# Kernel tuning notes

Measured on AMD Instinct MI355X. Metric: run time of the kernel, lower is better.

Reference implementation:

```python
import jax, jax.numpy as jnp
import numpy as np

B, F, H, LAT = 4, 64, 128, 512
N_CALLS = 16          # n_calls=2, module multiplies by 8
NEG = 0.2             # leaky-relu slope
EPS = 1e-5            # InstanceNorm2d eps

# hypernetwork output layout: w_in[F,3F], b_in[F], w_mid[F,F], b_mid[F], w_out[F,F], b_out[F], w_short[F,3F], b_short[F]
_sizes = [3*F*F, F, F*F, F, F*F, F, 3*F*F, F]
_off = np.cumsum([0] + _sizes)
HYP_OUT = int(_off[-1])


def _sobel_kernel():
    # SinSobel: smoothing (cos) x derivative (sin) separable 5x5 gradient filters
    lin = np.linspace(-1.0, 1.0, 5)
    d = np.sin(lin * np.pi / 2.0)
    s = np.cos(lin * np.pi / 2.0)
    gx = np.outer(s, d)                      # d/dx
    gy = np.outer(d, s)                      # d/dy
    k = np.stack([gx, gy])[:, None]          # [2,1,5,5]
    return jnp.asarray(np.tile(k, (F, 1, 1, 1)), jnp.float32)  # [2F,1,5,5] depthwise


def _conv(x, w, pad, groups=1):
    return jax.lax.conv_general_dilated(
        x, w, (1, 1), [(pad, pad), (pad, pad)],
        dimension_numbers=('NCHW', 'OIHW', 'NCHW'),
        feature_group_count=groups)


def _lrelu(x):
    return jnp.where(x >= 0, x, NEG * x)


def setup_inputs() -> dict:
    key = jax.random.key(0)
    ks = jax.random.split(key, 8)
    f32 = jnp.float32
    return {
        "lat": jax.random.normal(ks[0], (B, LAT), f32),
        "ca_init": jax.random.normal(ks[1], (B, F, H, H), f32),
        "leak_factor": jnp.asarray(0.1, f32),
        "hyper_w": jax.random.normal(ks[2], (HYP_OUT, LAT), f32) * 0.02,
        "hyper_b": jnp.zeros((HYP_OUT,), f32),
        "res_w1": jax.random.normal(ks[3], (F, F, 3, 3), f32) * 0.05,
        "res_b1": jnp.zeros((F,), f32),
        "res_w2": jax.random.normal(ks[4], (F, F, 3, 3), f32) * 0.05,
        "res_b2": jnp.zeros((F,), f32),
        "img_w": jax.random.normal(ks[5], (3, F, 3, 3), f32) * 0.05,
        "img_b": jnp.zeros((3,), f32),
    }


def reference(lat, ca_init, leak_factor, hyper_w, hyper_b,
              res_w1, res_b1, res_w2, res_b2, img_w, img_b):
    sob = _sobel_kernel()
    lf = jnp.clip(leak_factor, 0.001, 1000.0)

    # per-sample dynamic 1x1-conv weights from hypernetwork (lat is loop-invariant)
    ws = lat @ hyper_w.T + hyper_b           # [B, HYP_OUT]

    def seg(i, shape):
        return ws[:, _off[i]:_off[i + 1]].reshape((B,) + shape)
    w_in,  b_in  = seg(0, (F, 3 * F)), seg(1, (F,))
    w_mid, b_mid = seg(2, (F, F)),     seg(3, (F,))
    w_out, b_out = seg(4, (F, F)),     seg(5, (F,))
    w_sh,  b_sh  = seg(6, (F, 3 * F)), seg(7, (F,))

    def step(out, _):
        # SinSobel: identity channels + depthwise 5x5 gradients -> [B,3F,H,H]
        y = jnp.concatenate([out, _conv(out, sob, 2, groups=F)], axis=1)
        # InstanceNorm2d (affine=False)
        mu = y.mean((2, 3), keepdims=True)
        var = y.var((2, 3), keepdims=True)
        y = (y - mu) * jax.lax.rsqrt(var + EPS)
        # DynaResidualBlock: per-sample 1x1 convs (batched GEMMs) + shortcut
        h = _lrelu(jnp.einsum('bchw,boc->bohw', y, w_in) + b_in[:, :, None, None])
        h = _lrelu(jnp.einsum('bchw,boc->bohw', h, w_mid) + b_mid[:, :, None, None])
        h = jnp.einsum('bchw,boc->bohw', h, w_out) + b_out[:, :, None, None]
        sc = jnp.einsum('bchw,boc->bohw', y, w_sh) + b_sh[:, :, None, None]
        return out + lf * (h + sc), None

    out, _ = jax.lax.scan(step, ca_init, None, length=N_CALLS)

    # conv_img: ResidualBlock(3x3) then final 3x3 conv to image channels, clamp
    h = _lrelu(_conv(out, res_w1, 1) + res_b1[None, :, None, None])
    h = _conv(h, res_w2, 1) + res_b2[None, :, None, None]
    out = out + h
    img = _conv(out, img_w, 1) + img_b[None, :, None, None]
    return jnp.clip(img, -1.0, 1.0)
```

## Files before the change

kernel.cpp:

```cpp
#include <hip/hip_runtime.h>
#include <cstddef>

#define R_ 0.70710678118654752f
#define NEG_ 0.2f
#define EPS_ 1e-5f

constexpr int F_ = 64, C3_ = 192, HH_ = 128, NPIX_ = 16384, B_ = 4, LAT_ = 512, HYP_ = 33024;
constexpr int OFFI_WIN = 0, OFFI_BIN = 12288, OFFI_WMID = 12352, OFFI_BMID = 16448,
              OFFI_WOUT = 16512, OFFI_BOUT = 20608, OFFI_WSH = 20672, OFFI_BSH = 32960;
constexpr size_t OFF_HYP = 0;
constexpr size_t OFF_SRAW = 134144;
constexpr size_t OFF_WFIN = 140288;
constexpr size_t OFF_WFSH = 189440;
constexpr size_t OFF_WFMID = 238592;
constexpr size_t OFF_WFOUT = 254976;
constexpr size_t OFF_CW1 = 271360;
constexpr size_t OFF_CW2 = 308224;
constexpr size_t OFF_CWIMG = 345088;
constexpr size_t OFF_OUT = 346816;
constexpr size_t OFF_SOB = 4541120;
constexpr size_t OFF_TMP = OFF_SOB;

typedef short bf16x8 __attribute__((ext_vector_type(8)));
typedef float f32x4 __attribute__((ext_vector_type(4)));

static __device__ __forceinline__ unsigned short f2b(float v) {
  unsigned u = __builtin_bit_cast(unsigned, v);
  u += 0x7fffu + ((u >> 16) & 1u);
  return (unsigned short)(u >> 16);
}
static __device__ __forceinline__ float b2f(unsigned short h) {
  return __builtin_bit_cast(float, ((unsigned)h) << 16);
}
static __device__ __forceinline__ void split2(float v, unsigned short& hi, unsigned short& lo) {
  hi = f2b(v);
  lo = f2b(v - b2f(hi));
}

#define MM3(acc, ahi, alo, whi, wlo)                                        \
  acc = __builtin_amdgcn_mfma_f32_16x16x32_bf16(ahi, whi, acc, 0, 0, 0);    \
  acc = __builtin_amdgcn_mfma_f32_16x16x32_bf16(ahi, wlo, acc, 0, 0, 0);    \
  acc = __builtin_amdgcn_mfma_f32_16x16x32_bf16(alo, whi, acc, 0, 0, 0);

__global__ __launch_bounds__(256) void hyper_gemm_kernel(
    const float* __restrict__ lat, const float* __restrict__ hw,
    const float* __restrict__ hb, float* __restrict__ hyp) {
  __shared__ float slat[B_ * LAT_];
  const int tid = threadIdx.x;
  for (int i = tid; i < B_ * LAT_; i += 256) slat[i] = lat[i];
  __syncthreads();
  const int wave = tid >> 6, lane = tid & 63;
  const int j = blockIdx.x * 4 + wave;
  if (j >= HYP_) return;
  const float* wr = hw + (size_t)j * LAT_;
  float a0 = 0.f, a1 = 0.f, a2 = 0.f, a3 = 0.f;
  for (int i = 0; i < LAT_; i += 64) {
    float w = wr[i + lane];
    a0 = __builtin_fmaf(w, slat[0 * LAT_ + i + lane], a0);
    a1 = __builtin_fmaf(w, slat[1 * LAT_ + i + lane], a1);
    a2 = __builtin_fmaf(w, slat[2 * LAT_ + i + lane], a2);
    a3 = __builtin_fmaf(w, slat[3 * LAT_ + i + lane], a3);
  }
  #pragma unroll
  for (int off = 32; off; off >>= 1) {
    a0 += __shfl_down(a0, off, 64);
    a1 += __shfl_down(a1, off, 64);
    a2 += __shfl_down(a2, off, 64);
    a3 += __shfl_down(a3, off, 64);
  }
  if (lane == 0) {
    float b = hb[j];
    hyp[0 * HYP_ + j] = a0 + b;
    hyp[1 * HYP_ + j] = a1 + b;
    hyp[2 * HYP_ + j] = a2 + b;
    hyp[3 * HYP_ + j] = a3 + b;
  }
}

__global__ __launch_bounds__(256) void prep_dynw_kernel(float* wsm) {
  const int b = blockIdx.x >> 3, sl = blockIdx.x & 7;
  const int tid = threadIdx.x;
  const float* hyp = wsm + OFF_HYP + (size_t)b * HYP_;
  unsigned short* wfin = (unsigned short*)(wsm + OFF_WFIN) + (size_t)b * 24576;
  unsigned short* wfsh = (unsigned short*)(wsm + OFF_WFSH) + (size_t)b * 24576;
  unsigned short* wfmid = (unsigned short*)(wsm + OFF_WFMID) + (size_t)b * 8192;
  unsigned short* wfout = (unsigned short*)(wsm + OFF_WFOUT) + (size_t)b * 8192;

  if (sl < 6) {
    const int base = sl * 2048;
    for (int i = tid; i < 2048; i += 256) {
      int idx = base + i;
      int j = idx & 7, ch = (idx >> 3) & 63, g2 = (idx >> 9) & 3, ks = idx >> 11;
      int k = ks * 32 + g2 * 8 + j;
      int fbx = ((ks * 4 + g2) * 64 + ch) * 16;
      unsigned short h, l;
      split2(hyp[OFFI_WIN + ch * C3_ + k], h, l);
      wfin[fbx + j] = h; wfin[fbx + 8 + j] = l;
      split2(hyp[OFFI_WSH + ch * C3_ + k], h, l);
      wfsh[fbx + j] = h; wfsh[fbx + 8 + j] = l;
    }
  } else if (sl == 6) {
    for (int idx = tid; idx < 4096; idx += 256) {
      int j = idx & 7, ch = (idx >> 3) & 63, g2 = (idx >> 9) & 3, ks = idx >> 11;
      int k = ks * 32 + g2 * 8 + j;
      int fbx = ((ks * 4 + g2) * 64 + ch) * 16;
      unsigned short h, l;
      split2(hyp[OFFI_WMID + ch * 64 + k], h, l);
      wfmid[fbx + j] = h; wfmid[fbx + 8 + j] = l;
      split2(hyp[OFFI_WOUT + ch * 64 + k], h, l);
      wfout[fbx + j] = h; wfout[fbx + 8 + j] = l;
    }
  }
}

__global__ __launch_bounds__(256) void prep_convw_kernel(
    const float* __restrict__ w1, const float* __restrict__ w2,
    const float* __restrict__ wi, unsigned short* __restrict__ wf1,
    unsigned short* __restrict__ wf2, float* __restrict__ wit) {
  const int idx = blockIdx.x * 256 + threadIdx.x;
  if (idx < 36864) {
    int j = idx & 7, ch = (idx >> 3) & 63, fg = idx >> 9;
    int k = (fg >> 2) * 32 + (fg & 3) * 8 + j;
    int c = k & 63, t = k >> 6;
    int fb = (fg * 64 + ch) * 16;
    unsigned short h, l;
    split2(w1[(ch * 64 + c) * 9 + t], h, l);
    wf1[fb + j] = h; wf1[fb + 8 + j] = l;
    split2(w2[(ch * 64 + c) * 9 + t], h, l);
    wf2[fb + j] = h; wf2[fb + 8 + j] = l;
  }
  if (idx < 64 * 9 * 3) {
    int k = idx % 3, rest = idx / 3;
    int t = rest % 9, c = rest / 9;
    wit[idx] = wi[(k * 64 + c) * 9 + t];
  }
}

__device__ __forceinline__ float blockReduceSum(float v, float* scratch) {
  const int tid = threadIdx.x;
  #pragma unroll
  for (int off = 32; off; off >>= 1) v += __shfl_down(v, off, 64);
  if ((tid & 63) == 0) scratch[tid >> 6] = v;
  __syncthreads();
  float r = scratch[0] + scratch[1] + scratch[2] + scratch[3];
  __syncthreads();
  return r;
}

__device__ __forceinline__ void hline_z(const float* __restrict__ P, int rr, int col,
                                        float& hdv, float& hsv, float& cv) {
  if (rr < 0 || rr > 127) { hdv = 0.f; hsv = 0.f; cv = 0.f; return; }
  const float* rp = P + rr * HH_;
  float vm2 = (col >= 2) ? rp[col - 2] : 0.f;
  float vm1 = (col >= 1) ? rp[col - 1] : 0.f;
  float v0 = rp[col];
  float vp1 = (col <= 126) ? rp[col + 1] : 0.f;
  float vp2 = (col <= 125) ? rp[col + 2] : 0.f;
  hdv = -vm2 - R_ * vm1 + R_ * vp1 + vp2;
  hsv = R_ * vm1 + v0 + R_ * vp1;
  cv = v0;
}

__global__ __launch_bounds__(256) void sobel_stats_kernel(
    const float* __restrict__ outb, unsigned int* __restrict__ sob,
    float* __restrict__ sraw) {
  __shared__ float scr[4];
  const int bi = blockIdx.x;
  const int q = bi & 3, c = (bi >> 2) & 63, b = bi >> 8;
  const int tid = threadIdx.x;
  const int col = tid & 127;
  const int r0 = q * 32 + (tid >> 7) * 16;
  const float* P = outb + ((size_t)(b * F_ + c)) * NPIX_;
  unsigned int* ygx = sob + ((size_t)(b * 128 + 2 * c)) * NPIX_;
  unsigned int* ygy = ygx + NPIX_;

  float sI = 0.f, qI = 0.f, sX = 0.f, qX = 0.f, sY = 0.f, qY = 0.f;
  float hd_m1, hd_0, hd_p1, hs_m2, hs_m1, hs_0, hs_p1;
  float td, tc;
  hline_z(P, r0 - 2, col, td, hs_m2, tc);
  hline_z(P, r0 - 1, col, hd_m1, hs_m1, tc);
  hline_z(P, r0, col, hd_0, hs_0, tc);
  sI += tc; qI += tc * tc;
  hline_z(P, r0 + 1, col, hd_p1, hs_p1, tc);
  sI += tc; qI += tc * tc;

  for (int i = 0; i < 16; ++i) {
    const int r = r0 + i;
    const int nr = r + 2;
    float hd_new, hs_new, cnew;
    hline_z(P, nr, col, hd_new, hs_new, cnew);
    if (nr <= r0 + 15) { sI += cnew; qI += cnew * cnew; }
    float gxv = R_ * (hd_m1 + hd_p1) + hd_0;
    float gyv = -hs_m2 - R_ * hs_m1 + R_ * hs_p1 + hs_new;
    const int o = r * HH_ + col;
    unsigned short h, l;
    split2(gxv, h, l);
    ygx[o] = ((unsigned)h << 16) | l;
    split2(gyv, h, l);
    ygy[o] = ((unsigned)h << 16) | l;
    sX += gxv; qX += gxv * gxv;
    sY += gyv; qY += gyv * gyv;
    hd_m1 = hd_0; hd_0 = hd_p1; hd_p1 = hd_new;
    hs_m2 = hs_m1; hs_m1 = hs_0; hs_0 = hs_p1; hs_p1 = hs_new;
  }
  __syncthreads();
  float tI = blockReduceSum(sI, scr);
  float tQI = blockReduceSum(qI, scr);
  float tX = blockReduceSum(sX, scr);
  float tQX = blockReduceSum(qX, scr);
  float tY = blockReduceSum(sY, scr);
  float tQY = blockReduceSum(qY, scr);
  if (tid == 0) {
    float* r = sraw + (size_t)bi * 6;
    r[0] = tI; r[1] = tQI; r[2] = tX; r[3] = tQX; r[4] = tY; r[5] = tQY;
  }
}

__global__ __launch_bounds__(256, 2) void mlp_mfma_kernel(
    float* __restrict__ outb, const unsigned int* __restrict__ sobu,
    const float* __restrict__ wsf, const float* __restrict__ leak) {
  __shared__ unsigned short yhi[64 * 200];
  __shared__ unsigned short ylo[64 * 200];
  __shared__ unsigned short hhi[64 * 72];
  __shared__ unsigned short hlo[64 * 72];
  __shared__ unsigned short resb[64 * 66];
  __shared__ float stl[C3_ * 2];
  __shared__ float ssig[64];
  const int bi = blockIdx.x;
  const int b = bi >> 8, t = bi & 255;
  const int px0 = t * 64;
  const int tid = threadIdx.x;

  const float* ob = outb + (size_t)b * F_ * NPIX_;
  const unsigned int* sbp = sobu + (size_t)b * 128 * NPIX_;
  uint4 vbuf[12];
  #pragma unroll
  for (int it = 0; it < 12; ++it) {
    const int ci = it * 256 + tid;
    const int k = ci >> 4, pq = ci & 15;
    const unsigned int* src =
        (k < 64) ? (const unsigned int*)(ob + (size_t)k * NPIX_ + px0 + pq * 4)
                 : (sbp + (size_t)(k - 64) * NPIX_ + px0 + pq * 4);
    vbuf[it] = *(const uint4*)src;
  }

  if (tid < 64) {
    const int c = tid;
    const float* r = wsf + OFF_SRAW + ((size_t)(b * 64 + c) * 4) * 6;
    float sI = 0.f, qI = 0.f, sX = 0.f, qX = 0.f, sY = 0.f, qY = 0.f;
    #pragma unroll
    for (int q = 0; q < 4; ++q) {
      sI += r[q * 6 + 0]; qI += r[q * 6 + 1];
      sX += r[q * 6 + 2]; qX += r[q * 6 + 3];
      sY += r[q * 6 + 4]; qY += r[q * 6 + 5];
    }
    const float n = 1.f / 16384.f;
    float m, rs;
    m = sI * n; rs = rsqrtf(qI * n - m * m + EPS_);
    stl[c * 2] = m; stl[c * 2 + 1] = rs; ssig[c] = 1.f / rs;
    const int cx = 64 + 2 * c, cy = cx + 1;
    m = sX * n; stl[cx * 2] = m;          stl[cx * 2 + 1] = rsqrtf(qX * n - m * m + EPS_);
    m = sY * n; stl[cy * 2] = m;          stl[cy * 2 + 1] = rsqrtf(qY * n - m * m + EPS_);
  }
  __syncthreads();

  #pragma unroll
  for (int it = 0; it < 12; ++it) {
    const int ci = it * 256 + tid;
    const int k = ci >> 4, pq = ci & 15;
    const int kk = k ^ ((pq >> 1) << 3);
    unsigned short* ph = &yhi[(pq * 4) * 200 + kk];
    unsigned short* pl = &ylo[(pq * 4) * 200 + kk];
    const float mu = stl[k * 2], inv = stl[k * 2 + 1];
    const uint4 v = vbuf[it];
    if (k < 64) {
      const float sg = ssig[k];
      const float vv[4] = {__builtin_bit_cast(float, v.x), __builtin_bit_cast(float, v.y),
                           __builtin_bit_cast(float, v.z), __builtin_bit_cast(float, v.w)};
      #pragma unroll
      for (int e = 0; e < 4; ++e) {
        unsigned short h, l;
        split2((vv[e] - mu) * inv, h, l);
        ph[e * 200] = h; pl[e * 200] = l;
        float rec = __builtin_fmaf(b2f(h) + b2f(l), sg, mu);
        resb[k * 66 + pq * 4 + e] = f2b(vv[e] - rec);
      }
    } else {
      const unsigned uu[4] = {v.x, v.y, v.z, v.w};
      #pragma unroll
      for (int e = 0; e < 4; ++e) {
        float val = b2f((unsigned short)(uu[e] >> 16)) + b2f((unsigned short)(uu[e] & 0xffff));
        unsigned short h, l;
        split2((val - mu) * inv, h, l);
        ph[e * 200] = h; pl[e * 200] = l;
      }
    }
  }
  __syncthreads();

  const int wave = tid >> 6, lane = tid & 63;
  const int lrow = lane & 15, g = lane >> 4;
  const int chm = wave * 16 + lrow;
  const float lf = fminf(fmaxf(leak[0], 0.001f), 1000.f);
  const float* hyp = wsf + OFF_HYP + (size_t)b * HYP_;
  const unsigned short* wfin = (const unsigned short*)(wsf + OFF_WFIN) + (size_t)b * 24576;
  const unsigned short* wfsh = (const unsigned short*)(wsf + OFF_WFSH) + (size_t)b * 24576;
  const unsigned short* wfmid = (const unsigned short*)(wsf + OFF_WFMID) + (size_t)b * 8192;
  const unsigned short* wfout = (const unsigned short*)(wsf + OFF_WFOUT) + (size_t)b * 8192;

  f32x4 aH[4], aS[4];
  {
    float b1 = hyp[OFFI_BIN + chm], b2 = hyp[OFFI_BSH + chm];
    #pragma unroll
    for (int pf = 0; pf < 4; ++pf) {
      aH[pf] = (f32x4){b1, b1, b1, b1};
      aS[pf] = (f32x4){b2, b2, b2, b2};
    }
  }
  #pragma unroll
  for (int ks = 0; ks < 6; ++ks) {
    const size_t wo = (size_t)((ks * 4 + g) * 64 + chm) * 16;
    bf16x8 whiI = *(const bf16x8*)(wfin + wo);
    bf16x8 wloI = *(const bf16x8*)(wfin + wo + 8);
    bf16x8 whiS = *(const bf16x8*)(wfsh + wo);
    bf16x8 wloS = *(const bf16x8*)(wfsh + wo + 8);
    #pragma unroll
    for (int pf = 0; pf < 4; ++pf) {
      const int pxl = pf * 16 + lrow;
      const int kb = pxl * 200 + ((ks * 32 + g * 8) ^ ((pxl >> 3) << 3));
      bf16x8 ahi = *(const bf16x8*)&yhi[kb];
      bf16x8 alo = *(const bf16x8*)&ylo[kb];
      MM3(aH[pf], ahi, alo, whiI, wloI);
      MM3(aS[pf], ahi, alo, whiS, wloS);
    }
  }
  #pragma unroll
  for (int pf = 0; pf < 4; ++pf) {
    #pragma unroll
    for (int j = 0; j < 4; ++j) {
      float v = aH[pf][j];
      v = (v >= 0.f) ? v : NEG_ * v;
      unsigned short h, l;
      split2(v, h, l);
      const int o = (pf * 16 + g * 4 + j) * 72 + chm;
      hhi[o] = h; hlo[o] = l;
    }
  }
  __syncthreads();
  f32x4 aM[4];
  {
    float bm = hyp[OFFI_BMID + chm];
    #pragma unroll
    for (int pf = 0; pf < 4; ++pf) aM[pf] = (f32x4){bm, bm, bm, bm};
  }
  #pragma unroll
  for (int ks = 0; ks < 2; ++ks) {
    const size_t wo = (size_t)((ks * 4 + g) * 64 + chm) * 16;
    bf16x8 whi = *(const bf16x8*)(wfmid + wo);
    bf16x8 wlo = *(const bf16x8*)(wfmid + wo + 8);
    #pragma unroll
    for (int pf = 0; pf < 4; ++pf) {
      const int kb = (pf * 16 + lrow) * 72 + ks * 32 + g * 8;
      bf16x8 ahi = *(const bf16x8*)&hhi[kb];
      bf16x8 alo = *(const bf16x8*)&hlo[kb];
      MM3(aM[pf], ahi, alo, whi, wlo);
    }
  }
  __syncthreads();
  #pragma unroll
  for (int pf = 0; pf < 4; ++pf) {
    #pragma unroll
    for (int j = 0; j < 4; ++j) {
      float v = aM[pf][j];
      v = (v >= 0.f) ? v : NEG_ * v;
      unsigned short h, l;
      split2(v, h, l);
      const int o = (pf * 16 + g * 4 + j) * 72 + chm;
      hhi[o] = h; hlo[o] = l;
    }
  }
  __syncthreads();
  f32x4 aO[4];
  {
    float bo = hyp[OFFI_BOUT + chm];
    #pragma unroll
    for (int pf = 0; pf < 4; ++pf) aO[pf] = (f32x4){bo, bo, bo, bo};
  }
  #pragma unroll
  for (int ks = 0; ks < 2; ++ks) {
    const size_t wo = (size_t)((ks * 4 + g) * 64 + chm) * 16;
    bf16x8 whi = *(const bf16x8*)(wfout + wo);
    bf16x8 wlo = *(const bf16x8*)(wfout + wo + 8);
    #pragma unroll
    for (int pf = 0; pf < 4; ++pf) {
      const int kb = (pf * 16 + lrow) * 72 + ks * 32 + g * 8;
      bf16x8 ahi = *(const bf16x8*)&hhi[kb];
      bf16x8 alo = *(const bf16x8*)&hlo[kb];
      MM3(aO[pf], ahi, alo, whi, wlo);
    }
  }
  const float mu_c = stl[chm * 2];
  const float sg_c = ssig[chm];
  #pragma unroll
  for (int pf = 0; pf < 4; ++pf) {
    float* op = outb + ((size_t)(b * F_ + chm)) * NPIX_ + px0 + pf * 16 + g * 4;
    f32x4 nv;
    #pragma unroll
    for (int j = 0; j < 4; ++j) {
      const int pxl = pf * 16 + g * 4 + j;
      const int kk2 = chm ^ ((pxl >> 3) << 3);
      float yv = b2f(yhi[pxl * 200 + kk2]) + b2f(ylo[pxl * 200 + kk2]);
      float vorig = __builtin_fmaf(yv, sg_c, mu_c) + b2f(resb[chm * 66 + pxl]);
      nv[j] = vorig + lf * (aO[pf][j] + aS[pf][j]);
    }
    *(f32x4*)op = nv;
  }
}

__global__ __launch_bounds__(256, 2) void conv_mfma_kernel(
    const float* __restrict__ in, const unsigned short* __restrict__ wf,
    const float* __restrict__ bias, float* __restrict__ dst, int mode) {
  __shared__ unsigned short ahi[4 * 72 * 64];
  __shared__ unsigned short alo[4 * 72 * 64];
  const int bi = blockIdx.x;
  const int b = bi >> 7, rest = bi & 127;
  const int row0 = (rest >> 1) * 2, colbase = (rest & 1) << 6;
  const int tid = threadIdx.x;
  const float* ip = in + (size_t)b * F_ * NPIX_;

  for (int idx = tid; idx < 4608; idx += 256) {
    const int chunk = idx % 18;
    const int rowp = (idx / 18) % 4;
    const int ch = idx / 72;
    const int r2 = row0 - 1 + rowp;
    const int gcol0 = colbase - 4 + chunk * 4;
    float4 v;
    if (r2 < 0 || r2 > 127) {
      v = make_float4(0.f, 0.f, 0.f, 0.f);
    } else if (gcol0 >= 0 && gcol0 <= 124) {
      v = *(const float4*)(ip + (size_t)ch * NPIX_ + r2 * HH_ + gcol0);
    } else {
      const float* rp = ip + (size_t)ch * NPIX_ + r2 * HH_;
      v.x = (gcol0 >= 0 && gcol0 < 128) ? rp[gcol0] : 0.f;
      v.y = (gcol0 + 1 >= 0 && gcol0 + 1 < 128) ? rp[gcol0 + 1] : 0.f;
      v.z = (gcol0 + 2 >= 0 && gcol0 + 2 < 128) ? rp[gcol0 + 2] : 0.f;
      v.w = (gcol0 + 3 >= 0 && gcol0 + 3 < 128) ? rp[gcol0 + 3] : 0.f;
    }
    const float vv[4] = {v.x, v.y, v.z, v.w};
    #pragma unroll
    for (int e = 0; e < 4; ++e) {
      const int i = chunk * 4 + e;
      const int sw = (((i >> 2) & 7) ^ ((i & 3) << 1) ^ rowp) << 3;
      const int a = (rowp * 72 + i) * 64 + (ch ^ sw);
      unsigned short h, l;
      split2(vv[e], h, l);
      ahi[a] = h; alo[a] = l;
    }
  }
  __syncthreads();

  const int wave = tid >> 6, lane = tid & 63;
  const int lrow = lane & 15, g = lane >> 4;
  const int pxl = wave * 16 + lrow;
  f32x4 acc0[4], acc1[4];
  #pragma unroll
  for (int cg = 0; cg < 4; ++cg) {
    float bz = bias[cg * 16 + lrow];
    acc0[cg] = (f32x4){bz, bz, bz, bz};
    acc1[cg] = (f32x4){bz, bz, bz, bz};
  }
  for (int ks = 0; ks < 18; ++ks) {
    const int kbase = ks * 32 + g * 8;
    const int t = kbase >> 6, c0 = kbase & 63;
    const int dy = t / 3 - 1, dx = t % 3 - 1;
    const int i = pxl + 4 + dx;
    const int rp0 = 1 + dy, rp1 = 2 + dy;
    const int sw0 = (((i >> 2) & 7) ^ ((i & 3) << 1) ^ rp0) << 3;
    const int sw1 = (((i >> 2) & 7) ^ ((i & 3) << 1) ^ rp1) << 3;
    const int a0 = (rp0 * 72 + i) * 64 + (c0 ^ sw0);
    const int a1 = (rp1 * 72 + i) * 64 + (c0 ^ sw1);
    bf16x8 ah0 = *(const bf16x8*)&ahi[a0];
    bf16x8 al0 = *(const bf16x8*)&alo[a0];
    bf16x8 ah1 = *(const bf16x8*)&ahi[a1];
    bf16x8 al1 = *(const bf16x8*)&alo[a1];
    #pragma unroll
    for (int cg = 0; cg < 4; ++cg) {
      const unsigned short* wp = wf + (size_t)((ks * 4 + g) * 64 + cg * 16 + lrow) * 16;
      bf16x8 whi = *(const bf16x8*)wp;
      bf16x8 wlo = *(const bf16x8*)(wp + 8);
      MM3(acc0[cg], ah0, al0, whi, wlo);
      MM3(acc1[cg], ah1, al1, whi, wlo);
    }
  }
  #pragma unroll
  for (int r = 0; r < 2; ++r) {
    #pragma unroll
    for (int cg = 0; cg < 4; ++cg) {
      const f32x4 av = r ? acc1[cg] : acc0[cg];
      float* op = dst + ((size_t)(b * F_ + cg * 16 + lrow)) * NPIX_ + (row0 + r) * HH_ +
                  colbase + wave * 16 + g * 4;
      if (mode == 1) {
        f32x4 rr;
        #pragma unroll
        for (int j = 0; j < 4; ++j) {
          float v = av[j];
          rr[j] = (v >= 0.f) ? v : NEG_ * v;
        }
        *(f32x4*)op = rr;
      } else {
        f32x4 cur = *(f32x4*)op;
        #pragma unroll
        for (int j = 0; j < 4; ++j) cur[j] += av[j];
        *(f32x4*)op = cur;
      }
    }
  }
}

__global__ __launch_bounds__(256, 4) void convimg_kernel(
    const float* __restrict__ outb, const float* __restrict__ wT,
    const float* __restrict__ bias, float* __restrict__ img) {
  __shared__ float part[2 * 128 * 3];
  const int bi = blockIdx.x;
  const int b = bi >> 7, pxb = bi & 127;
  const int tid = threadIdx.x;
  const int px = tid & 127;
  const int hf = __builtin_amdgcn_readfirstlane(tid >> 7);
  const int p = pxb * 128 + px;
  const int row = p >> 7, col = p & 127;
  float a0 = 0.f, a1 = 0.f, a2 = 0.f;
  const float* ip = outb + (size_t)b * F_ * NPIX_;
  for (int cc = 0; cc < 32; ++cc) {
    const int c = hf * 32 + cc;
    const float* pl = ip + (size_t)c * NPIX_;
    #pragma unroll
    for (int t = 0; t < 9; ++t) {
      const int dy = t / 3 - 1, dx = t % 3 - 1;
      const int r2 = row + dy, c2 = col + dx;
      float v = (r2 >= 0 && r2 < 128 && c2 >= 0 && c2 < 128) ? pl[r2 * HH_ + c2] : 0.f;
      const float* wp = wT + (c * 9 + t) * 3;
      a0 = __builtin_fmaf(v, wp[0], a0);
      a1 = __builtin_fmaf(v, wp[1], a1);
      a2 = __builtin_fmaf(v, wp[2], a2);
    }
  }
  part[(hf * 128 + px) * 3 + 0] = a0;
  part[(hf * 128 + px) * 3 + 1] = a1;
  part[(hf * 128 + px) * 3 + 2] = a2;
  __syncthreads();
  if (hf == 0) {
    float r0 = a0 + part[(128 + px) * 3 + 0] + bias[0];
    float r1 = a1 + part[(128 + px) * 3 + 1] + bias[1];
    float r2 = a2 + part[(128 + px) * 3 + 2] + bias[2];
    img[((size_t)b * 3 + 0) * NPIX_ + p] = fminf(fmaxf(r0, -1.f), 1.f);
    img[((size_t)b * 3 + 1) * NPIX_ + p] = fminf(fmaxf(r1, -1.f), 1.f);
    img[((size_t)b * 3 + 2) * NPIX_ + p] = fminf(fmaxf(r2, -1.f), 1.f);
  }
}

extern "C" void kernel_launch(void* const* d_in, const int* in_sizes, int n_in,
                              void* d_out, int out_size, void* d_ws, size_t ws_size,
                              hipStream_t stream) {
  const float* lat = (const float*)d_in[0];
  const float* ca_init = (const float*)d_in[1];
  const float* leak = (const float*)d_in[2];
  const float* hyper_w = (const float*)d_in[3];
  const float* hyper_b = (const float*)d_in[4];
  const float* res_w1 = (const float*)d_in[5];
  const float* res_b1 = (const float*)d_in[6];
  const float* res_w2 = (const float*)d_in[7];
  const float* res_b2 = (const float*)d_in[8];
  const float* img_w = (const float*)d_in[9];
  const float* img_b = (const float*)d_in[10];
  float* out = (float*)d_out;
  float* ws = (float*)d_ws;
  unsigned int* sobu = (unsigned int*)(ws + OFF_SOB);

  hyper_gemm_kernel<<<(HYP_ + 3) / 4, 256, 0, stream>>>(lat, hyper_w, hyper_b, ws + OFF_HYP);
  prep_dynw_kernel<<<32, 256, 0, stream>>>(ws);
  prep_convw_kernel<<<144, 256, 0, stream>>>(res_w1, res_w2, img_w,
                                             (unsigned short*)(ws + OFF_CW1),
                                             (unsigned short*)(ws + OFF_CW2),
                                             ws + OFF_CWIMG);
  hipMemcpyAsync(ws + OFF_OUT, ca_init, (size_t)B_ * F_ * NPIX_ * sizeof(float),
                 hipMemcpyDeviceToDevice, stream);

  for (int st = 0; st < 16; ++st) {
    sobel_stats_kernel<<<1024, 256, 0, stream>>>(ws + OFF_OUT, sobu, ws + OFF_SRAW);
    mlp_mfma_kernel<<<1024, 256, 0, stream>>>(ws + OFF_OUT, sobu, ws, leak);
  }

  conv_mfma_kernel<<<512, 256, 0, stream>>>(ws + OFF_OUT, (const unsigned short*)(ws + OFF_CW1),
                                            res_b1, (float*)(ws + OFF_TMP), 1);
  conv_mfma_kernel<<<512, 256, 0, stream>>>((const float*)(ws + OFF_TMP),
                                            (const unsigned short*)(ws + OFF_CW2),
                                            res_b2, ws + OFF_OUT, 2);
  convimg_kernel<<<512, 256, 0, stream>>>(ws + OFF_OUT, ws + OFF_CWIMG, img_b, out);
}
```

Baseline: 945.5 us.

## Double sobel block threads with shorter row strips; load MLP inputs after stats

The sobel/stats kernel now runs 512 threads per block, each handling 8 rows instead of 16, with an 8-wave block reduction. This adds parallelism and latency hiding at the cost of more halo-row reloads per thread. In the MLP kernel, the 12 prefetched uint4 loads into registers are replaced by loads inside the normalization loop after the stats barrier. That lowers register pressure but gives up the early prefetch that overlapped with the stats computation.

After: 879.8 us. 7.0% less time.

```diff
diff --git a/kernel.cpp b/kernel.cpp
--- a/kernel.cpp
+++ b/kernel.cpp
@@ -136,17 +136,6 @@
   }
 }
 
-__device__ __forceinline__ float blockReduceSum(float v, float* scratch) {
-  const int tid = threadIdx.x;
-  #pragma unroll
-  for (int off = 32; off; off >>= 1) v += __shfl_down(v, off, 64);
-  if ((tid & 63) == 0) scratch[tid >> 6] = v;
-  __syncthreads();
-  float r = scratch[0] + scratch[1] + scratch[2] + scratch[3];
-  __syncthreads();
-  return r;
-}
-
 __device__ __forceinline__ void hline_z(const float* __restrict__ P, int rr, int col,
                                         float& hdv, float& hsv, float& cv) {
   if (rr < 0 || rr > 127) { hdv = 0.f; hsv = 0.f; cv = 0.f; return; }
@@ -161,15 +150,28 @@
   cv = v0;
 }
 
-__global__ __launch_bounds__(256) void sobel_stats_kernel(
+__device__ __forceinline__ float blockReduceSum8(float v, float* scratch) {
+  const int tid = threadIdx.x;
+  #pragma unroll
+  for (int off = 32; off; off >>= 1) v += __shfl_down(v, off, 64);
+  if ((tid & 63) == 0) scratch[tid >> 6] = v;
+  __syncthreads();
+  float r = 0.f;
+  #pragma unroll
+  for (int w = 0; w < 8; ++w) r += scratch[w];
+  __syncthreads();
+  return r;
+}
+
+__global__ __launch_bounds__(512) void sobel_stats_kernel(
     const float* __restrict__ outb, unsigned int* __restrict__ sob,
     float* __restrict__ sraw) {
-  __shared__ float scr[4];
+  __shared__ float scr[8];
   const int bi = blockIdx.x;
   const int q = bi & 3, c = (bi >> 2) & 63, b = bi >> 8;
   const int tid = threadIdx.x;
   const int col = tid & 127;
-  const int r0 = q * 32 + (tid >> 7) * 16;
+  const int r0 = q * 32 + (tid >> 7) * 8;
   const float* P = outb + ((size_t)(b * F_ + c)) * NPIX_;
   unsigned int* ygx = sob + ((size_t)(b * 128 + 2 * c)) * NPIX_;
   unsigned int* ygy = ygx + NPIX_;
@@ -184,12 +186,12 @@
   hline_z(P, r0 + 1, col, hd_p1, hs_p1, tc);
   sI += tc; qI += tc * tc;
 
-  for (int i = 0; i < 16; ++i) {
+  for (int i = 0; i < 8; ++i) {
     const int r = r0 + i;
     const int nr = r + 2;
     float hd_new, hs_new, cnew;
     hline_z(P, nr, col, hd_new, hs_new, cnew);
-    if (nr <= r0 + 15) { sI += cnew; qI += cnew * cnew; }
+    if (nr <= r0 + 7) { sI += cnew; qI += cnew * cnew; }
     float gxv = R_ * (hd_m1 + hd_p1) + hd_0;
     float gyv = -hs_m2 - R_ * hs_m1 + R_ * hs_p1 + hs_new;
     const int o = r * HH_ + col;
@@ -204,12 +206,12 @@
     hs_m2 = hs_m1; hs_m1 = hs_0; hs_0 = hs_p1; hs_p1 = hs_new;
   }
   __syncthreads();
-  float tI = blockReduceSum(sI, scr);
-  float tQI = blockReduceSum(qI, scr);
-  float tX = blockReduceSum(sX, scr);
-  float tQX = blockReduceSum(qX, scr);
-  float tY = blockReduceSum(sY, scr);
-  float tQY = blockReduceSum(qY, scr);
+  float tI = blockReduceSum8(sI, scr);
+  float tQI = blockReduceSum8(qI, scr);
+  float tX = blockReduceSum8(sX, scr);
+  float tQX = blockReduceSum8(qX, scr);
+  float tY = blockReduceSum8(sY, scr);
+  float tQY = blockReduceSum8(qY, scr);
   if (tid == 0) {
     float* r = sraw + (size_t)bi * 6;
     r[0] = tI; r[1] = tQI; r[2] = tX; r[3] = tQX; r[4] = tY; r[5] = tQY;
@@ -231,19 +233,6 @@
   const int px0 = t * 64;
   const int tid = threadIdx.x;
 
-  const float* ob = outb + (size_t)b * F_ * NPIX_;
-  const unsigned int* sbp = sobu + (size_t)b * 128 * NPIX_;
-  uint4 vbuf[12];
-  #pragma unroll
-  for (int it = 0; it < 12; ++it) {
-    const int ci = it * 256 + tid;
-    const int k = ci >> 4, pq = ci & 15;
-    const unsigned int* src =
-        (k < 64) ? (const unsigned int*)(ob + (size_t)k * NPIX_ + px0 + pq * 4)
-                 : (sbp + (size_t)(k - 64) * NPIX_ + px0 + pq * 4);
-    vbuf[it] = *(const uint4*)src;
-  }
-
   if (tid < 64) {
     const int c = tid;
     const float* r = wsf + OFF_SRAW + ((size_t)(b * 64 + c) * 4) * 6;
@@ -264,19 +253,21 @@
   }
   __syncthreads();
 
+  const float* ob = outb + (size_t)b * F_ * NPIX_;
+  const unsigned int* sbp = sobu + (size_t)b * 128 * NPIX_;
   #pragma unroll
   for (int it = 0; it < 12; ++it) {
-    const int ci = it * 256 + tid;
-    const int k = ci >> 4, pq = ci & 15;
-    const int kk = k ^ ((pq >> 1) << 3);
+    int ci = it * 256 + tid;
+    int k = ci >> 4, pq = ci & 15;
+    int kk = k ^ ((pq >> 1) << 3);
     unsigned short* ph = &yhi[(pq * 4) * 200 + kk];
     unsigned short* pl = &ylo[(pq * 4) * 200 + kk];
     const float mu = stl[k * 2], inv = stl[k * 2 + 1];
-    const uint4 v = vbuf[it];
+    float vv[4];
     if (k < 64) {
+      float4 f = *(const float4*)(ob + (size_t)k * NPIX_ + px0 + pq * 4);
+      vv[0] = f.x; vv[1] = f.y; vv[2] = f.z; vv[3] = f.w;
       const float sg = ssig[k];
-      const float vv[4] = {__builtin_bit_cast(float, v.x), __builtin_bit_cast(float, v.y),
-                           __builtin_bit_cast(float, v.z), __builtin_bit_cast(float, v.w)};
       #pragma unroll
       for (int e = 0; e < 4; ++e) {
         unsigned short h, l;
@@ -286,12 +277,15 @@
         resb[k * 66 + pq * 4 + e] = f2b(vv[e] - rec);
       }
     } else {
-      const unsigned uu[4] = {v.x, v.y, v.z, v.w};
+      uint4 v = *(const uint4*)(sbp + (size_t)(k - 64) * NPIX_ + px0 + pq * 4);
+      vv[0] = b2f((unsigned short)(v.x >> 16)) + b2f((unsigned short)(v.x & 0xffff));
+      vv[1] = b2f((unsigned short)(v.y >> 16)) + b2f((unsigned short)(v.y & 0xffff));
+      vv[2] = b2f((unsigned short)(v.z >> 16)) + b2f((unsigned short)(v.z & 0xffff));
+      vv[3] = b2f((unsigned short)(v.w >> 16)) + b2f((unsigned short)(v.w & 0xffff));
       #pragma unroll
       for (int e = 0; e < 4; ++e) {
-        float val = b2f((unsigned short)(uu[e] >> 16)) + b2f((unsigned short)(uu[e] & 0xffff));
         unsigned short h, l;
-        split2((val - mu) * inv, h, l);
+        split2((vv[e] - mu) * inv, h, l);
         ph[e * 200] = h; pl[e * 200] = l;
       }
     }
@@ -586,7 +580,7 @@
                  hipMemcpyDeviceToDevice, stream);
 
   for (int st = 0; st < 16; ++st) {
-    sobel_stats_kernel<<<1024, 256, 0, stream>>>(ws + OFF_OUT, sobu, ws + OFF_SRAW);
+    sobel_stats_kernel<<<1024, 512, 0, stream>>>(ws + OFF_OUT, sobu, ws + OFF_SRAW);
     mlp_mfma_kernel<<<1024, 256, 0, stream>>>(ws + OFF_OUT, sobu, ws, leak);
   }
 
```
